# Kernel tuning notes

Measured on AMD Instinct MI355X. Metric: run time of the kernel, lower is better.

The kernel has to match this reference:

```python
import jax, jax.numpy as jnp
import numpy as np

I, H, B, T = 17, 128, 32768, 19

def setup_inputs() -> dict:
    key = jax.random.key(0)
    ks = jax.random.split(key, 7)
    s = 1.0 / np.sqrt(H)  # PyTorch LSTMCell/Linear init scale
    u = lambda k, shape: jax.random.uniform(k, shape, jnp.float32, -s, s)
    return {
        "x": jax.random.normal(ks[0], (B, T, I), jnp.float32),
        "W_ih": u(ks[1], (4 * H, I)),
        "W_hh": u(ks[2], (4 * H, H)),
        "b_ih": u(ks[3], (4 * H,)),
        "b_hh": u(ks[4], (4 * H,)),
        "W_out": u(ks[5], (I, H)),
        "b_out": u(ks[6], (I,)),
    }

def reference(x, W_ih, W_hh, b_ih, b_hh, W_out, b_out):
    B_, T_, _ = x.shape
    Hh = W_hh.shape[1]
    # Precompute input projections for all timesteps in one GEMM: [B,T,4H]
    x_proj = jnp.einsum('bti,gi->btg', x, W_ih) + b_ih + b_hh

    def step(carry, xp_t):
        h, c = carry
        gates = xp_t + h @ W_hh.T            # [B,4H]
        i_g, f_g, g_g, o_g = jnp.split(gates, 4, axis=-1)
        c = jax.nn.sigmoid(f_g) * c + jax.nn.sigmoid(i_g) * jnp.tanh(g_g)
        h = jax.nn.sigmoid(o_g) * jnp.tanh(c)
        y = h @ W_out.T + b_out              # [B,I]
        return (h, c), y

    h0 = jnp.zeros((B_, Hh), x.dtype)
    c0 = jnp.zeros((B_, Hh), x.dtype)
    _, ys = jax.lax.scan(step, (h0, c0), jnp.swapaxes(x_proj, 0, 1))  # ys: [T,B,I]
    return jnp.swapaxes(ys, 0, 1)  # [B,T,I]
```

## Files before the change

### kernel.cpp

```cpp
#include <hip/hip_runtime.h>

#define I_DIM 17
#define H_DIM 128
#define T_DIM 19
#define B_DIM 32768
#define M_ROWS 64
#define NTHR 1024
#define GRID (B_DIM / M_ROWS)
#define XI 323
#define XSLOT 2176

#define OFF_WHH 0
#define OFF_H   131072
#define OFF_X   147456
#define OFF_WO  151808
#define LDS_TOT 160000

typedef __bf16 bf16x8 __attribute__((ext_vector_type(8)));
typedef float f32x4 __attribute__((ext_vector_type(4)));
typedef float f32x4u __attribute__((ext_vector_type(4), aligned(4)));
union FragU { bf16x8 v; unsigned short s[8]; uint4 u; };

#define K1 1.4426950408889634f
#define K2 2.8853900817779268f

__device__ __forceinline__ unsigned short f2bf(float f) {
    union { float f; unsigned u; } x; x.f = f;
    return (unsigned short)((x.u + 0x8000u) >> 16);
}

#define STEP_READ(P_, REC_) do {                                                  \
    _Pragma("unroll") for (int tile = 0; tile < 2; ++tile) {                      \
        FragU fx; fx.u = (uint4){0u, 0u, 0u, 0u};                                 \
        if (q < 2)                                                                \
            fx.v = *(const bf16x8*)(smem + xyA + ((P_) * XSLOT + tile * 512));    \
        else if (q == 2) {                                                        \
            fx.s[0] = *(const unsigned short*)(smem + xk16 + ((P_) * XSLOT + tile * 32)); \
            fx.s[1] = (unsigned short)0x3F80;                \
        }                                                                         \
        _Pragma("unroll") for (int g = 0; g < 4; ++g) {                           \
            f32x4 z = {0.f, 0.f, 0.f, 0.f};                                       \
            acc[tile][g] = __builtin_amdgcn_mfma_f32_16x16x32_bf16(wihr[g], fx.v, z, 0, 0, 0); \
        }                                                                         \
    }                                                                             \
    if (REC_) {                                                                   \
        _Pragma("unroll") for (int kk = 0; kk < 4; ++kk) {                        \
            bf16x8 aw[4];                                                         \
            _Pragma("unroll") for (int g = 0; g < 4; ++g)                         \
                aw[g] = *(const bf16x8*)(smem + vwhh + (kk * 4096 + g * 1024));   \
            _Pragma("unroll") for (int tile = 0; tile < 2; ++tile) {              \
                bf16x8 hb = *(const bf16x8*)(smem + vkk[kk] + tile * 4096);       \
                _Pragma("unroll") for (int g = 0; g < 4; ++g)                     \
                    acc[tile][g] = __builtin_amdgcn_mfma_f32_16x16x32_bf16(aw[g], hb, acc[tile][g], 0, 0, 0); \
            }                                                                     \
        }                                                                         \
    }                                                                             \
} while (0)

#define ELEM_T(TILE_) do {                                                        \
    unsigned long long hp = 0ull;                                                 \
    _Pragma("unroll") for (int r = 0; r < 4; ++r) {                               \
        float ui = __builtin_amdgcn_exp2f(acc[TILE_][0][r]);                      \
        float uf = __builtin_amdgcn_exp2f(acc[TILE_][1][r]);                      \
        float vg = __builtin_amdgcn_exp2f(acc[TILE_][2][r]);                      \
        float uo = __builtin_amdgcn_exp2f(acc[TILE_][3][r]);                      \
        float A_ = 1.f + ui, F_ = 1.f + uf, G_ = 1.f + vg;                        \
        float AG = A_ * G_;                                                       \
        int ci = (TILE_) * 4 + r;                                                 \
        float c = (cst[ci] * AG + (1.f - vg) * F_) * __builtin_amdgcn_rcpf(F_ * AG); \
        cst[ci] = c;                                                              \
        float vc = __builtin_amdgcn_exp2f(-K2 * c);                               \
        float h = (1.f - vc) * __builtin_amdgcn_rcpf((1.f + uo) * (1.f + vc));    \
        union { float f; unsigned u; } hu; hu.f = h;                              \
        hp |= (unsigned long long)((hu.u + 0x8000u) >> 16) << (16 * r);           \
    }                                                                             \
    *(unsigned long long*)(smem + vwrT + (TILE_) * 4096) = hp;                    \
} while (0)

#define Y_BURST() do {                                                            \
    if (w < 8) {                                                                  \
        f32x4 ya = {0.f, 0.f, 0.f, 0.f};                                          \
        _Pragma("unroll") for (int kk = 0; kk < 4; ++kk) {                        \
            bf16x8 wa = *(const bf16x8*)(smem + vwo + kk * 1024);                 \
            bf16x8 hb = *(const bf16x8*)(smem + yv[kk]);                          \
            ya = __builtin_amdgcn_mfma_f32_16x16x32_bf16(wa, hb, ya, 0, 0, 0);    \
        }                                                                         \
        if (yct == 0) {                                                           \
            *(f32x4u*)ypt = ya + ybo;                                             \
        } else if (q == 0) {                                                      \
            ypt[0] = ya[0] + ybo[0];                                              \
        }                                                                         \
        ypt += I_DIM;                                                             \
    }                                                                             \
} while (0)

#define STEP(T_, P_, REC_) do {                                                   \
    float xr1 = 0.f, xr2 = 0.f;                                                   \
    const bool pf = (T_) + 1 < T_DIM;                                             \
    if (pf) { xr1 = xp1[17]; if (xv2) xr2 = xp2[17]; }                            \
    xp1 += 17; xp2 += 17;                                                         \
    STEP_READ(P_, REC_);                                                          \
    if (REC_) { Y_BURST(); __syncthreads(); }                \
    ELEM_T(0); ELEM_T(1);                                                         \
    if (pf) {                                                                     \
        *(unsigned short*)(smem + xd1 + (1 - (P_)) * XSLOT) = f2bf(xr1);          \
        if (xv2) *(unsigned short*)(smem + xd2 + (1 - (P_)) * XSLOT) = f2bf(xr2); \
    }                                                                             \
    __syncthreads();                                \
} while (0)

__global__ __launch_bounds__(NTHR)
__attribute__((amdgpu_waves_per_eu(4, 4)))
void flowlstm(
    const float* __restrict__ x, const float* __restrict__ W_ih,
    const float* __restrict__ W_hh, const float* __restrict__ b_ih,
    const float* __restrict__ b_hh, const float* __restrict__ W_out,
    const float* __restrict__ b_out, float* __restrict__ out)
{
    __shared__ __align__(16) unsigned char smem[LDS_TOT];
    const int tid = threadIdx.x;
    const int w = tid >> 6, lane = tid & 63, l15 = lane & 15, q = lane >> 4;
    const int mh = w >> 3, cg = w & 7;
    const int b0 = blockIdx.x * M_ROWS;

    #pragma unroll
    for (int i = 0; i < 8; ++i) {
        int s = tid + i * NTHR;
        int ln = s & 63, f = s >> 6;
        int g = f & 3, kk = (f >> 2) & 3, cgs = f >> 4;
        float sc = (g == 2) ? -K2 : -K1;
        int n = g * H_DIM + cgs * 16 + (ln & 15);
        const float* sp = W_hh + n * H_DIM + kk * 32 + (ln >> 4) * 8;
        FragU fu;
        #pragma unroll
        for (int e = 0; e < 8; ++e) fu.s[e] = f2bf(sp[e] * sc);
        *(uint4*)(smem + OFF_WHH + f * 1024 + ln * 16) = fu.u;
    }
    if (tid < 512) {
        int ln = tid & 63, f = tid >> 6;
        int kk = f & 3, ct = f >> 2;
        int o = ct * 16 + (ln & 15);
        int kb = kk * 32 + (ln >> 4) * 8;
        FragU fu;
        #pragma unroll
        for (int e = 0; e < 8; ++e)
            fu.s[e] = (o < I_DIM) ? f2bf(W_out[o * H_DIM + kb + e]) : (unsigned short)0;
        *(uint4*)(smem + OFF_WO + f * 1024 + ln * 16) = fu.u;
    }
    bf16x8 wihr[4];
    #pragma unroll
    for (int g = 0; g < 4; ++g) {
        float sc = (g == 2) ? -K2 : -K1;
        int n = g * H_DIM + cg * 16 + l15;
        FragU fu;
        #pragma unroll
        for (int e = 0; e < 8; ++e) {
            int k = q * 8 + e;
            float v = 0.f;
            if (k < I_DIM)       v = W_ih[n * I_DIM + k] * sc;
            else if (k == I_DIM) v = (b_ih[n] + b_hh[n]) * sc;
            fu.s[e] = f2bf(v);
        }
        wihr[g] = fu.v;
    }
    const unsigned xr7 = (unsigned)((l15 & 7) << 4);
    unsigned vkk[4], yv[4];
    #pragma unroll
    for (int kk = 0; kk < 4; ++kk)
        vkk[kk] = (unsigned)(OFF_H + mh * 8192 + l15 * 256 + ((kk * 64 + q * 16) ^ xr7));
    const unsigned vwrT = (unsigned)(OFF_H + mh * 8192 + l15 * 256 + (((cg * 16 + 4 * q) * 2) ^ xr7));
    const unsigned vwhh = (unsigned)(OFF_WHH + cg * 16384 + lane * 16);
    const int yct = w & 1;
    const unsigned ytile = (unsigned)((w >> 1) * 4096);
    #pragma unroll
    for (int kk = 0; kk < 4; ++kk)
        yv[kk] = (unsigned)(OFF_H + ytile + l15 * 256 + ((kk * 64 + q * 16) ^ xr7));
    const unsigned vwo = (unsigned)(OFF_WO + yct * 4096 + lane * 16);
    f32x4 ybo;
    #pragma unroll
    for (int r = 0; r < 4; ++r) {
        int col = yct * 16 + 4 * q + r;
        ybo[r] = b_out[col < I_DIM ? col : 16];
    }
    const unsigned xyA  = (unsigned)(OFF_X + mh * 1024 + (q < 2 ? q * 256 : 0) + l15 * 16);
    const unsigned xk16 = (unsigned)(OFF_X + 2048 + mh * 64 + l15 * 2);
    float* ypt = out + (size_t)(b0 + (w >> 1) * 16 + l15) * XI + (yct ? 16 : 4 * q);

    const unsigned row1 = ((unsigned)tid * 61681u) >> 20;
    const unsigned k1 = (unsigned)tid - row1 * 17u;
    const bool xv2 = tid < (M_ROWS * I_DIM - NTHR);
    const unsigned f2v = (unsigned)(tid + NTHR);
    const unsigned row2 = xv2 ? ((f2v * 61681u) >> 20) : 0u;
    const unsigned k2 = xv2 ? (f2v - row2 * 17u) : 0u;
    const unsigned xd1 = (k1 == 16) ? (unsigned)(OFF_X + 2048 + row1 * 2)
        : (unsigned)(OFF_X + (row1 >> 4) * 512 + (k1 >> 3) * 256 + (row1 & 15) * 16 + (k1 & 7) * 2);
    const unsigned xd2 = (k2 == 16) ? (unsigned)(OFF_X + 2048 + row2 * 2)
        : (unsigned)(OFF_X + (row2 >> 4) * 512 + (k2 >> 3) * 256 + (row2 & 15) * 16 + (k2 & 7) * 2);
    const float* xp1 = x + (size_t)(b0 + row1) * XI + k1;
    const float* xp2 = x + (size_t)(b0 + row2) * XI + k2;

    *(unsigned short*)(smem + xd1) = f2bf(xp1[0]);
    if (xv2) *(unsigned short*)(smem + xd2) = f2bf(xp2[0]);

    float cst[8];
    #pragma unroll
    for (int i = 0; i < 8; ++i) cst[i] = 0.f;

    f32x4 acc[2][4];

    __syncthreads();

    STEP(0, 0, 0);

    #pragma unroll 1
    for (int t = 1; t < T_DIM; t += 2) {
        STEP(t, 1, 1);
        STEP(t + 1, 0, 1);
    }

    if (w < 8) {
        f32x4 ya = {0.f, 0.f, 0.f, 0.f};
        #pragma unroll
        for (int kk = 0; kk < 4; ++kk) {
            bf16x8 wa = *(const bf16x8*)(smem + vwo + kk * 1024);
            bf16x8 hb = *(const bf16x8*)(smem + yv[kk]);
            ya = __builtin_amdgcn_mfma_f32_16x16x32_bf16(wa, hb, ya, 0, 0, 0);
        }
        if (yct == 0) {
            *(f32x4u*)ypt = ya + ybo;
        } else if (q == 0) {
            ypt[0] = ya[0] + ybo[0];
        }
    }
}

extern "C" void kernel_launch(void* const* d_in, const int* in_sizes, int n_in,
                              void* d_out, int out_size, void* d_ws, size_t ws_size,
                              hipStream_t stream) {
    const float* x     = (const float*)d_in[0];
    const float* W_ih  = (const float*)d_in[1];
    const float* W_hh  = (const float*)d_in[2];
    const float* b_ih  = (const float*)d_in[3];
    const float* b_hh  = (const float*)d_in[4];
    const float* W_out = (const float*)d_in[5];
    const float* b_out = (const float*)d_in[6];
    float* out = (float*)d_out;

    dim3 grid(GRID), block(NTHR);
    flowlstm<<<grid, block, 0, stream>>>(x, W_ih, W_hh, b_ih, b_hh, W_out, b_out, out);
}
```

Before: 160.5 us.

## Ping-pong two wave groups so matrix and elementwise phases overlap across row halves

Splits the 16 waves into two groups, each owning an independent 32-row half of the batch tile. The groups alternate phases so one runs the gate MFMAs while the other runs the sigmoid/tanh elementwise work, with the x staging and output projection moved into the elementwise slots. W_out is now held in registers instead of LDS, which frees LDS but raises register pressure. The schedule is hand-interleaved and takes more barrier phases per timestep, so correctness depends on the phase ordering being exact.

```diff
diff --git a/kernel.cpp b/kernel.cpp
--- a/kernel.cpp
+++ b/kernel.cpp
@@ -13,8 +13,7 @@
 #define OFF_WHH 0
 #define OFF_H   131072
 #define OFF_X   147456
-#define OFF_WO  151808
-#define LDS_TOT 160000
+#define LDS_TOT 151808
 
 typedef __bf16 bf16x8 __attribute__((ext_vector_type(8)));
 typedef float f32x4 __attribute__((ext_vector_type(4)));
@@ -29,18 +28,18 @@
     return (unsigned short)((x.u + 0x8000u) >> 16);
 }
 
-#define STEP_READ(P_, REC_) do {                                                  \
-    _Pragma("unroll") for (int tile = 0; tile < 2; ++tile) {                      \
+#define MFMA_G(XP_, REC_, DOY_) do {                                              \
+    _Pragma("unroll") for (int m = 0; m < 2; ++m) {                               \
         FragU fx; fx.u = (uint4){0u, 0u, 0u, 0u};                                 \
         if (q < 2)                                                                \
-            fx.v = *(const bf16x8*)(smem + xyA + ((P_) * XSLOT + tile * 512));    \
+            fx.v = *(const bf16x8*)(smem + vxy + ((XP_) * XSLOT + m * 512));      \
         else if (q == 2) {                                                        \
-            fx.s[0] = *(const unsigned short*)(smem + xk16 + ((P_) * XSLOT + tile * 32)); \
-            fx.s[1] = (unsigned short)0x3F80;                \
+            fx.s[0] = *(const unsigned short*)(smem + vx16 + ((XP_) * XSLOT + m * 32)); \
+            fx.s[1] = (unsigned short)0x3F80;                                     \
         }                                                                         \
         _Pragma("unroll") for (int g = 0; g < 4; ++g) {                           \
             f32x4 z = {0.f, 0.f, 0.f, 0.f};                                       \
-            acc[tile][g] = __builtin_amdgcn_mfma_f32_16x16x32_bf16(wihr[g], fx.v, z, 0, 0, 0); \
+            acc[m][g] = __builtin_amdgcn_mfma_f32_16x16x32_bf16(wihr[g], fx.v, z, 0, 0, 0); \
         }                                                                         \
     }                                                                             \
     if (REC_) {                                                                   \
@@ -48,65 +47,59 @@
             bf16x8 aw[4];                                                         \
             _Pragma("unroll") for (int g = 0; g < 4; ++g)                         \
                 aw[g] = *(const bf16x8*)(smem + vwhh + (kk * 4096 + g * 1024));   \
-            _Pragma("unroll") for (int tile = 0; tile < 2; ++tile) {              \
-                bf16x8 hb = *(const bf16x8*)(smem + vkk[kk] + tile * 4096);       \
+            _Pragma("unroll") for (int m = 0; m < 2; ++m) {                       \
+                bf16x8 hb = *(const bf16x8*)(smem + vkk[kk] + m * 4096);          \
                 _Pragma("unroll") for (int g = 0; g < 4; ++g)                     \
-                    acc[tile][g] = __builtin_amdgcn_mfma_f32_16x16x32_bf16(aw[g], hb, acc[tile][g], 0, 0, 0); \
+                    acc[m][g] = __builtin_amdgcn_mfma_f32_16x16x32_bf16(aw[g], hb, acc[m][g], 0, 0, 0); \
             }                                                                     \
         }                                                                         \
     }                                                                             \
-} while (0)
-
-#define ELEM_T(TILE_) do {                                                        \
-    unsigned long long hp = 0ull;                                                 \
-    _Pragma("unroll") for (int r = 0; r < 4; ++r) {                               \
-        float ui = __builtin_amdgcn_exp2f(acc[TILE_][0][r]);                      \
-        float uf = __builtin_amdgcn_exp2f(acc[TILE_][1][r]);                      \
-        float vg = __builtin_amdgcn_exp2f(acc[TILE_][2][r]);                      \
-        float uo = __builtin_amdgcn_exp2f(acc[TILE_][3][r]);                      \
-        float A_ = 1.f + ui, F_ = 1.f + uf, G_ = 1.f + vg;                        \
-        float AG = A_ * G_;                                                       \
-        int ci = (TILE_) * 4 + r;                                                 \
-        float c = (cst[ci] * AG + (1.f - vg) * F_) * __builtin_amdgcn_rcpf(F_ * AG); \
-        cst[ci] = c;                                                              \
-        float vc = __builtin_amdgcn_exp2f(-K2 * c);                               \
-        float h = (1.f - vc) * __builtin_amdgcn_rcpf((1.f + uo) * (1.f + vc));    \
-        union { float f; unsigned u; } hu; hu.f = h;                              \
-        hp |= (unsigned long long)((hu.u + 0x8000u) >> 16) << (16 * r);           \
-    }                                                                             \
-    *(unsigned long long*)(smem + vwrT + (TILE_) * 4096) = hp;                    \
-} while (0)
-
-#define Y_BURST() do {                                                            \
-    if (w < 8) {                                                                  \
+    if (DOY_) Y_ONLY();                                                           \
+} while (0)
+
+#define Y_ONLY() do {                                                             \
+    if (yw) {                                                                     \
         f32x4 ya = {0.f, 0.f, 0.f, 0.f};                                          \
         _Pragma("unroll") for (int kk = 0; kk < 4; ++kk) {                        \
-            bf16x8 wa = *(const bf16x8*)(smem + vwo + kk * 1024);                 \
-            bf16x8 hb = *(const bf16x8*)(smem + yv[kk]);                          \
-            ya = __builtin_amdgcn_mfma_f32_16x16x32_bf16(wa, hb, ya, 0, 0, 0);    \
-        }                                                                         \
-        if (yct == 0) {                                                           \
-            *(f32x4u*)ypt = ya + ybo;                                             \
-        } else if (q == 0) {                                                      \
-            ypt[0] = ya[0] + ybo[0];                                              \
-        }                                                                         \
+            bf16x8 hb = *(const bf16x8*)(smem + vyv[kk]);                         \
+            ya = __builtin_amdgcn_mfma_f32_16x16x32_bf16(wor[kk], hb, ya, 0, 0, 0); \
+        }                                                                         \
+        if (yct == 0) { *(f32x4u*)ypt = ya + ybo; }                               \
+        else if (q == 0) { ypt[0] = ya[0] + ybo[0]; }                             \
         ypt += I_DIM;                                                             \
     }                                                                             \
 } while (0)
 
-#define STEP(T_, P_, REC_) do {                                                   \
-    float xr1 = 0.f, xr2 = 0.f;                                                   \
-    const bool pf = (T_) + 1 < T_DIM;                                             \
-    if (pf) { xr1 = xp1[17]; if (xv2) xr2 = xp2[17]; }                            \
-    xp1 += 17; xp2 += 17;                                                         \
-    STEP_READ(P_, REC_);                                                          \
-    if (REC_) { Y_BURST(); __syncthreads(); }                \
-    ELEM_T(0); ELEM_T(1);                                                         \
-    if (pf) {                                                                     \
-        *(unsigned short*)(smem + xd1 + (1 - (P_)) * XSLOT) = f2bf(xr1);          \
-        if (xv2) *(unsigned short*)(smem + xd2 + (1 - (P_)) * XSLOT) = f2bf(xr2); \
-    }                                                                             \
-    __syncthreads();                                \
+#define ELEM_G() do {                                                             \
+    _Pragma("unroll") for (int m = 0; m < 2; ++m) {                               \
+        unsigned long long hp = 0ull;                                             \
+        _Pragma("unroll") for (int r = 0; r < 4; ++r) {                           \
+            float ui = __builtin_amdgcn_exp2f(acc[m][0][r]);                      \
+            float uf = __builtin_amdgcn_exp2f(acc[m][1][r]);                      \
+            float vg = __builtin_amdgcn_exp2f(acc[m][2][r]);                      \
+            float uo = __builtin_amdgcn_exp2f(acc[m][3][r]);                      \
+            float A_ = 1.f + ui, F_ = 1.f + uf, G_ = 1.f + vg;                    \
+            float AG = A_ * G_;                                                   \
+            int ci = m * 4 + r;                                                   \
+            float c = (cst[ci] * AG + (1.f - vg) * F_) * __builtin_amdgcn_rcpf(F_ * AG); \
+            cst[ci] = c;                                                          \
+            float vc = __builtin_amdgcn_exp2f(-K2 * c);                           \
+            float h = (1.f - vc) * __builtin_amdgcn_rcpf((1.f + uo) * (1.f + vc));\
+            union { float f; unsigned u; } hu; hu.f = h;                          \
+            hp |= (unsigned long long)((hu.u + 0x8000u) >> 16) << (16 * r);       \
+        }                                                                         \
+        *(unsigned long long*)(smem + vwrT + m * 4096) = hp;                      \
+    }                                                                             \
+} while (0)
+
+#define STAGE(XP_) do {                                                           \
+    float v1 = xs1[0];                                                            \
+    float v2 = xs2[0];                                                            \
+    float v3 = sv3 ? xs3[0] : 0.f;                                                \
+    xs1 += I_DIM; xs2 += I_DIM; xs3 += I_DIM;                                     \
+    *(unsigned short*)(smem + xd1 + (XP_) * XSLOT) = f2bf(v1);                    \
+    *(unsigned short*)(smem + xd2 + (XP_) * XSLOT) = f2bf(v2);                    \
+    if (sv3) *(unsigned short*)(smem + xd3 + (XP_) * XSLOT) = f2bf(v3);           \
 } while (0)
 
 __global__ __launch_bounds__(NTHR)
@@ -120,7 +113,9 @@
     __shared__ __align__(16) unsigned char smem[LDS_TOT];
     const int tid = threadIdx.x;
     const int w = tid >> 6, lane = tid & 63, l15 = lane & 15, q = lane >> 4;
-    const int mh = w >> 3, cg = w & 7;
+    const int grp = w >> 3;
+    const bool isG1 = (grp == 1);
+    const int cg = w & 7;
     const int b0 = blockIdx.x * M_ROWS;
 
     #pragma unroll
@@ -135,17 +130,6 @@
         #pragma unroll
         for (int e = 0; e < 8; ++e) fu.s[e] = f2bf(sp[e] * sc);
         *(uint4*)(smem + OFF_WHH + f * 1024 + ln * 16) = fu.u;
-    }
-    if (tid < 512) {
-        int ln = tid & 63, f = tid >> 6;
-        int kk = f & 3, ct = f >> 2;
-        int o = ct * 16 + (ln & 15);
-        int kb = kk * 32 + (ln >> 4) * 8;
-        FragU fu;
-        #pragma unroll
-        for (int e = 0; e < 8; ++e)
-            fu.s[e] = (o < I_DIM) ? f2bf(W_out[o * H_DIM + kb + e]) : (unsigned short)0;
-        *(uint4*)(smem + OFF_WO + f * 1024 + ln * 16) = fu.u;
     }
     bf16x8 wihr[4];
     #pragma unroll
@@ -163,75 +147,95 @@
         }
         wihr[g] = fu.v;
     }
+    const bool yw = (cg < 4);
+    const int yrt = (w >> 1) & 1, yct = w & 1;
+    const int ycol = yct * 16 + 4 * q;
+    bf16x8 wor[4];
+    #pragma unroll
+    for (int kk = 0; kk < 4; ++kk) {
+        int o = yct * 16 + l15;
+        FragU fu;
+        #pragma unroll
+        for (int e = 0; e < 8; ++e)
+            fu.s[e] = (o < I_DIM) ? f2bf(W_out[o * H_DIM + kk * 32 + q * 8 + e])
+                                  : (unsigned short)0;
+        wor[kk] = fu.v;
+    }
+    f32x4 ybo;
+    #pragma unroll
+    for (int r = 0; r < 4; ++r) {
+        int col = ycol + r;
+        ybo[r] = b_out[col < I_DIM ? col : 16];
+    }
     const unsigned xr7 = (unsigned)((l15 & 7) << 4);
-    unsigned vkk[4], yv[4];
-    #pragma unroll
-    for (int kk = 0; kk < 4; ++kk)
-        vkk[kk] = (unsigned)(OFF_H + mh * 8192 + l15 * 256 + ((kk * 64 + q * 16) ^ xr7));
-    const unsigned vwrT = (unsigned)(OFF_H + mh * 8192 + l15 * 256 + (((cg * 16 + 4 * q) * 2) ^ xr7));
+    const unsigned hbase = (unsigned)(OFF_H + grp * 8192);
+    unsigned vkk[4], vyv[4];
+    #pragma unroll
+    for (int kk = 0; kk < 4; ++kk) {
+        unsigned sw = (unsigned)((kk * 64 + q * 16) ^ xr7);
+        vkk[kk] = hbase + (unsigned)(l15 * 256) + sw;
+        vyv[kk] = hbase + (unsigned)(yrt * 4096 + l15 * 256) + sw;
+    }
+    const unsigned vwrT = hbase + (unsigned)(l15 * 256 + (((cg * 16 + 4 * q) * 2) ^ xr7));
     const unsigned vwhh = (unsigned)(OFF_WHH + cg * 16384 + lane * 16);
-    const int yct = w & 1;
-    const unsigned ytile = (unsigned)((w >> 1) * 4096);
-    #pragma unroll
-    for (int kk = 0; kk < 4; ++kk)
-        yv[kk] = (unsigned)(OFF_H + ytile + l15 * 256 + ((kk * 64 + q * 16) ^ xr7));
-    const unsigned vwo = (unsigned)(OFF_WO + yct * 4096 + lane * 16);
-    f32x4 ybo;
-    #pragma unroll
-    for (int r = 0; r < 4; ++r) {
-        int col = yct * 16 + 4 * q + r;
-        ybo[r] = b_out[col < I_DIM ? col : 16];
-    }
-    const unsigned xyA  = (unsigned)(OFF_X + mh * 1024 + (q < 2 ? q * 256 : 0) + l15 * 16);
-    const unsigned xk16 = (unsigned)(OFF_X + 2048 + mh * 64 + l15 * 2);
-    float* ypt = out + (size_t)(b0 + (w >> 1) * 16 + l15) * XI + (yct ? 16 : 4 * q);
-
-    const unsigned row1 = ((unsigned)tid * 61681u) >> 20;
-    const unsigned k1 = (unsigned)tid - row1 * 17u;
-    const bool xv2 = tid < (M_ROWS * I_DIM - NTHR);
-    const unsigned f2v = (unsigned)(tid + NTHR);
-    const unsigned row2 = xv2 ? ((f2v * 61681u) >> 20) : 0u;
-    const unsigned k2 = xv2 ? (f2v - row2 * 17u) : 0u;
-    const unsigned xd1 = (k1 == 16) ? (unsigned)(OFF_X + 2048 + row1 * 2)
-        : (unsigned)(OFF_X + (row1 >> 4) * 512 + (k1 >> 3) * 256 + (row1 & 15) * 16 + (k1 & 7) * 2);
-    const unsigned xd2 = (k2 == 16) ? (unsigned)(OFF_X + 2048 + row2 * 2)
-        : (unsigned)(OFF_X + (row2 >> 4) * 512 + (k2 >> 3) * 256 + (row2 & 15) * 16 + (k2 & 7) * 2);
-    const float* xp1 = x + (size_t)(b0 + row1) * XI + k1;
-    const float* xp2 = x + (size_t)(b0 + row2) * XI + k2;
-
-    *(unsigned short*)(smem + xd1) = f2bf(xp1[0]);
-    if (xv2) *(unsigned short*)(smem + xd2) = f2bf(xp2[0]);
+    const unsigned vxy  = (unsigned)(OFF_X + grp * 1024 + (q < 2 ? q * 256 : 0) + l15 * 16);
+    const unsigned vx16 = (unsigned)(OFF_X + 2048 + grp * 64 + l15 * 2);
+    float* ypt = out + (size_t)(b0 + grp * 32 + yrt * 16 + l15) * XI + (yct ? 16 : 4 * q);
+
+    const int g_tid = tid & 511;
+    const unsigned e1 = (unsigned)g_tid, e2 = e1 + 512u, e3 = e1 + 1024u;
+    const bool sv3 = (g_tid < 64);
+    const unsigned r1 = (e1 * 61681u) >> 20, k1v = e1 - r1 * 17u;
+    const unsigned r2 = (e2 * 61681u) >> 20, k2v = e2 - r2 * 17u;
+    const unsigned r3 = (e3 * 61681u) >> 20, k3v = e3 - r3 * 17u;
+    const unsigned xd1 = (k1v == 16u) ? (unsigned)(OFF_X + 2048 + r1 * 2)
+        : (unsigned)(OFF_X + (r1 >> 4) * 512 + (k1v >> 3) * 256 + (r1 & 15) * 16 + (k1v & 7) * 2);
+    const unsigned xd2 = (k2v == 16u) ? (unsigned)(OFF_X + 2048 + r2 * 2)
+        : (unsigned)(OFF_X + (r2 >> 4) * 512 + (k2v >> 3) * 256 + (r2 & 15) * 16 + (k2v & 7) * 2);
+    const unsigned xd3 = (k3v == 16u) ? (unsigned)(OFF_X + 2048 + r3 * 2)
+        : (unsigned)(OFF_X + (r3 >> 4) * 512 + (k3v >> 3) * 256 + (r3 & 15) * 16 + (k3v & 7) * 2);
+    const float* xs1 = x + (size_t)(b0 + r1) * XI + k1v;
+    const float* xs2 = x + (size_t)(b0 + r2) * XI + k2v;
+    const float* xs3 = x + (size_t)(b0 + r3) * XI + k3v;
 
     float cst[8];
     #pragma unroll
     for (int i = 0; i < 8; ++i) cst[i] = 0.f;
-
     f32x4 acc[2][4];
 
-    __syncthreads();
-
-    STEP(0, 0, 0);
+    if (isG1) STAGE(0);
+    __syncthreads();
+
+    if (!isG1) MFMA_G(0, 0, 0);
+    else       STAGE(1);
+    __syncthreads();
+
+    if (!isG1) ELEM_G(); else MFMA_G(0, 0, 0);
+    __syncthreads();
+    if (!isG1) MFMA_G(1, 1, 1); else { ELEM_G(); STAGE(0); }
+    __syncthreads();
 
     #pragma unroll 1
-    for (int t = 1; t < T_DIM; t += 2) {
-        STEP(t, 1, 1);
-        STEP(t + 1, 0, 1);
-    }
-
-    if (w < 8) {
-        f32x4 ya = {0.f, 0.f, 0.f, 0.f};
-        #pragma unroll
-        for (int kk = 0; kk < 4; ++kk) {
-            bf16x8 wa = *(const bf16x8*)(smem + vwo + kk * 1024);
-            bf16x8 hb = *(const bf16x8*)(smem + yv[kk]);
-            ya = __builtin_amdgcn_mfma_f32_16x16x32_bf16(wa, hb, ya, 0, 0, 0);
-        }
-        if (yct == 0) {
-            *(f32x4u*)ypt = ya + ybo;
-        } else if (q == 0) {
-            ypt[0] = ya[0] + ybo[0];
-        }
-    }
+    for (int p = 0; p < 8; ++p) {
+        if (!isG1) ELEM_G(); else MFMA_G(1, 1, 1);
+        __syncthreads();
+        if (!isG1) MFMA_G(0, 1, 1); else { ELEM_G(); STAGE(1); }
+        __syncthreads();
+        if (!isG1) ELEM_G(); else MFMA_G(0, 1, 1);
+        __syncthreads();
+        if (!isG1) MFMA_G(1, 1, 1); else { ELEM_G(); STAGE(0); }
+        __syncthreads();
+    }
+
+    if (!isG1) ELEM_G(); else MFMA_G(1, 1, 1);
+    __syncthreads();
+    if (!isG1) MFMA_G(0, 1, 1); else ELEM_G();
+    __syncthreads();
+    if (!isG1) ELEM_G(); else MFMA_G(0, 1, 1);
+    __syncthreads();
+    if (!isG1) { Y_ONLY(); } else ELEM_G();
+    __syncthreads();
+    if (isG1) Y_ONLY();
 }
 
 extern "C" void kernel_launch(void* const* d_in, const int* in_sizes, int n_in,
```

Result: slower. 186.6 us (+16.2%).
